# Optimization experiments

Hardware: AMD Instinct MI355X
Metric: run time of the kernel (lower is better)

Reference implementation:

```python
import jax, jax.numpy as jnp
import numpy as np

N, E = 20000, 160000
H, C1, C_OUT, D_IN = 4, 256, 512, 128
HID = H * C1  # 1024


def gat_conv(x, src, dst, W, a_src, a_dst, b, heads, ch, concat):
    n = x.shape[0]
    xw = (x @ W).reshape(n, heads, ch)                     # [N,H,C]
    es = jnp.sum(xw * a_src, axis=-1)                      # [N,H]
    ed = jnp.sum(xw * a_dst, axis=-1)                      # [N,H]
    e = jax.nn.leaky_relu(es[src] + ed[dst], 0.2)          # [Etot,H]
    m = jax.ops.segment_max(e, dst, num_segments=n)
    m = jnp.where(jnp.isfinite(m), m, 0.0)
    p = jnp.exp(e - m[dst])
    denom = jax.ops.segment_sum(p, dst, num_segments=n)
    alpha = p / (denom[dst] + 1e-16)                       # segment softmax
    out = jax.ops.segment_sum(alpha[:, :, None] * xw[src], dst, num_segments=n)
    out = out.reshape(n, heads * ch) if concat else out.mean(axis=1)
    return out + b


def layer_norm(x, g, b, eps=1e-5):
    mu = jnp.mean(x, axis=-1, keepdims=True)
    var = jnp.var(x, axis=-1, keepdims=True)
    return (x - mu) * jax.lax.rsqrt(var + eps) * g + b


def setup_inputs() -> dict:
    key = jax.random.key(0)
    ks = jax.random.split(key, 16)
    s1, s2, s3 = (2.0 / D_IN) ** 0.5, (2.0 / HID) ** 0.5, (2.0 / HID) ** 0.5
    return {
        "x": jax.random.normal(ks[0], (N, D_IN), jnp.float32),
        "edge_index": jax.random.randint(ks[1], (2, E), 0, N, jnp.int64),
        "W1": jax.random.normal(ks[2], (D_IN, H * C1), jnp.float32) * s1,
        "a_src1": jax.random.normal(ks[3], (H, C1), jnp.float32) * 0.1,
        "a_dst1": jax.random.normal(ks[4], (H, C1), jnp.float32) * 0.1,
        "b1": jnp.zeros((HID,), jnp.float32),
        "ln1_g": jnp.ones((HID,), jnp.float32),
        "ln1_b": jnp.zeros((HID,), jnp.float32),
        "W2": jax.random.normal(ks[5], (HID, H * C1), jnp.float32) * s2,
        "a_src2": jax.random.normal(ks[6], (H, C1), jnp.float32) * 0.1,
        "a_dst2": jax.random.normal(ks[7], (H, C1), jnp.float32) * 0.1,
        "b2": jnp.zeros((HID,), jnp.float32),
        "ln2_g": jnp.ones((HID,), jnp.float32),
        "ln2_b": jnp.zeros((HID,), jnp.float32),
        "W3": jax.random.normal(ks[8], (HID, C_OUT), jnp.float32) * s3,
        "a_src3": jax.random.normal(ks[9], (1, C_OUT), jnp.float32) * 0.1,
        "a_dst3": jax.random.normal(ks[10], (1, C_OUT), jnp.float32) * 0.1,
        "b3": jnp.zeros((C_OUT,), jnp.float32),
    }


def reference(x, edge_index, W1, a_src1, a_dst1, b1, ln1_g, ln1_b,
              W2, a_src2, a_dst2, b2, ln2_g, ln2_b,
              W3, a_src3, a_dst3, b3):
    # add self loops (PyG GATConv default add_self_loops=True)
    loops = jnp.arange(N, dtype=edge_index.dtype)
    src = jnp.concatenate([edge_index[0], loops])
    dst = jnp.concatenate([edge_index[1], loops])

    h = gat_conv(x, src, dst, W1, a_src1, a_dst1, b1, H, C1, True)
    h = jax.nn.elu(layer_norm(h, ln1_g, ln1_b))  # dropout: eval mode (identity)
    h = gat_conv(h, src, dst, W2, a_src2, a_dst2, b2, H, C1, True)
    h = jax.nn.elu(layer_norm(h, ln2_g, ln2_b))
    out = gat_conv(h, src, dst, W3, a_src3, a_dst3, b3, 1, C_OUT, True)
    return out
```

## Files before the change

kernel.cpp:

```cpp
#include <hip/hip_runtime.h>
#include <hip/hip_bf16.h>

typedef __hip_bfloat16 bf16;
typedef __attribute__((ext_vector_type(8))) short short8;
typedef __attribute__((ext_vector_type(8))) unsigned short ushort8v;
typedef __attribute__((ext_vector_type(4))) float float4v;

#define NN 20000
#define EE 160000
#define ET (NN + EE)

__device__ __forceinline__ float bf2f(bf16 v){ return __bfloat162float(v); }
__device__ __forceinline__ float raw2f(unsigned short u){ return __uint_as_float(((unsigned)u) << 16); }
__device__ __forceinline__ unsigned short f2raw(float f){
  bf16 h = __float2bfloat16(f);
  return *(unsigned short*)&h;
}

__device__ __forceinline__ int detect_f32(const void* raw, int nwords, int lane){
  unsigned v = ((const unsigned*)raw)[lane % nwords];
  int e8 = (v >> 7) & 0xFF;
  int looks = (e8 >= 100 && e8 <= 140) ? 1 : 0;
  unsigned long long mz = __ballot(v == 0u);
  unsigned long long ml = __ballot(looks);
  int nz = __popcll(mz);
  int nonz = 64 - nz;
  int nl = __popcll(ml);
  return (nonz > 0 && 2*nl >= nonz) ? 0 : 1;
}

__device__ __forceinline__ int detect_i64(const int* eiraw, int lane){
  int odd = eiraw[2*lane + 1];
  unsigned long long m2 = __ballot(odd != 0);
  return (m2 == 0ULL) ? 1 : 0;
}

struct P13 { const void* src[13]; int off[13]; int n[13]; };
struct PrepArgs {
  const void* xraw; bf16* Xc;
  const void* w1raw; bf16* Wt1;
  const void* w2raw; bf16* Wt2;
  const void* w3raw; bf16* Wt3;
  const int* eiraw; int* eic;
  P13 p13; float* prm;
  int* counts;
  float* esA; float* edA;
};

__device__ __forceinline__ void do_transpose(float (*tile)[33], const void* raw,
    bf16* wt, int K, int M, int f, int bx, int by, int t){
  int kb = by*32, mb = bx*32;
  int tx = t & 31, ty = t >> 5;
  for (int r = 0; r < 4; r++){
    int k = kb + ty + r*8;
    int m = mb + tx;
    float v = f ? ((const float*)raw)[(size_t)k*M+m] : bf2f(((const bf16*)raw)[(size_t)k*M+m]);
    tile[ty + r*8][tx] = v;
  }
  __syncthreads();
  for (int r = 0; r < 4; r++){
    int m = mb + ty + r*8;
    int k = kb + tx;
    wt[(size_t)m*K + k] = __float2bfloat16(tile[tx][ty + r*8]);
  }
}

__global__ __launch_bounds__(256) void k_prep(PrepArgs A){
  __shared__ float tile[32][33];
  int b = blockIdx.x, t = threadIdx.x;
  int lane = t & 63;
  if (b < 10000){
    int f = detect_f32(A.xraw, NN*128/2, lane);
    int i = b*256 + t;
    if (f) A.Xc[i] = __float2bfloat16(((const float*)A.xraw)[i]);
    else   A.Xc[i] = ((const bf16*)A.xraw)[i];
  } else if (b < 10128){
    int f = detect_f32(A.w1raw, 128*1024/2, lane);
    int r = b - 10000;
    do_transpose(tile, A.w1raw, A.Wt1, 128, 1024, f, r & 31, r >> 5, t);
  } else if (b < 11152){
    int f = detect_f32(A.w2raw, 1024*1024/2, lane);
    int r = b - 10128;
    do_transpose(tile, A.w2raw, A.Wt2, 1024, 1024, f, r & 31, r >> 5, t);
  } else if (b < 11664){
    int f = detect_f32(A.w3raw, 1024*512/2, lane);
    int r = b - 11152;
    do_transpose(tile, A.w3raw, A.Wt3, 1024, 512, f, r & 15, r >> 4, t);
  } else if (b < 12914){
    int f64 = detect_i64(A.eiraw, lane);
    int i = (b - 11664)*256 + t;
    if (i < 2*EE) A.eic[i] = f64 ? A.eiraw[2*i] : A.eiraw[i];
  } else if (b < 12927){
    int pb = b - 12914;
    const void* s = A.p13.src[pb];
    int n = A.p13.n[pb];
    int f = detect_f32(s, n/2, lane);
    float* d = A.prm + A.p13.off[pb];
    for (int i = t; i < n; i += 256)
      d[i] = f ? ((const float*)s)[i] : bf2f(((const bf16*)s)[i]);
  } else if (b < 13006){
    int i = (b - 12927)*256 + t;
    if (i < NN) A.counts[i] = 1;
  } else {
    int i = (b - 13006)*256 + t;
    if (i < NN*4){ A.esA[i] = 0.f; A.edA[i] = 0.f; }
  }
}

__global__ void k_hist(const int* __restrict__ ei, int* __restrict__ counts){
  int e = blockIdx.x*256 + threadIdx.x;
  if (e < EE){
    int d = ei[EE + e];
    if (d >= 0 && d < NN) atomicAdd(&counts[d], 1);
  }
}

__global__ __launch_bounds__(1024) void k_scan(const int* __restrict__ counts, int* __restrict__ rp,
    int* __restrict__ cursor, int* __restrict__ col){
  __shared__ int wsum[16];
  __shared__ int sc;
  int t = threadIdx.x, lane = t & 63, wv = t >> 6;
  if (t == 0) sc = 0;
  __syncthreads();
  for (int base = 0; base < NN; base += 1024){
    int i = base + t;
    int v = (i < NN) ? counts[i] : 0;
    int x = v;
    #pragma unroll
    for (int o = 1; o < 64; o <<= 1){
      int y = __shfl_up(x, o, 64);
      if (lane >= o) x += y;
    }
    if (lane == 63) wsum[wv] = x;
    __syncthreads();
    if (wv == 0 && lane < 16){
      int w = wsum[lane];
      #pragma unroll
      for (int o = 1; o < 16; o <<= 1){
        int y = __shfl_up(w, o, 16);
        if ((lane & 15) >= o) w += y;
      }
      wsum[lane] = w;
    }
    __syncthreads();
    int carry = sc;
    int wpre = (wv > 0) ? wsum[wv-1] : 0;
    if (i < NN){
      int p = carry + wpre + x - v;
      rp[i] = p;
      col[p] = i;
      cursor[i] = p + 1;
    }
    __syncthreads();
    if (t == 1023) sc = carry + wsum[15];
    __syncthreads();
  }
  if (t == 0) rp[NN] = sc;
}

__global__ void k_scatter(const int* __restrict__ ei, int* __restrict__ cursor, int* __restrict__ col){
  int e = blockIdx.x*256 + threadIdx.x;
  if (e < EE){
    int s = ei[e], d = ei[EE + e];
    if (d >= 0 && d < NN){
      int pos = atomicAdd(&cursor[d], 1);
      col[pos] = s;
    }
  }
}

__global__ __launch_bounds__(256) void k_gemm_mfma(
    const bf16* __restrict__ X, const bf16* __restrict__ Wt, bf16* __restrict__ Y,
    const float* __restrict__ as_, const float* __restrict__ ad_,
    float* __restrict__ es, float* __restrict__ ed,
    int K, int M, int C, int H)
{
  __shared__ bf16 Xs[64*64];
  __shared__ bf16 Bs[128*64];
  int ncols = gridDim.x;
  int bid = blockIdx.y * ncols + blockIdx.x;
  int xcd  = bid & 7;
  int rest = bid >> 3;
  int colb = rest % ncols;
  int rowb = xcd + 8 * (rest / ncols);
  int r0 = rowb * 64;
  if (r0 >= NN) return;
  int c0 = colb * 128;

  int tid  = threadIdx.x;
  int wave = tid >> 6, lane = tid & 63;
  int quad = lane >> 4, l15 = lane & 15;
  int wr = (wave >> 1) * 32;
  int wc = (wave & 1) * 64;
  int sw = l15 & 7;

  float4v acc[2][4];
  #pragma unroll
  for (int i=0;i<2;i++)
    #pragma unroll
    for (int j=0;j<4;j++)
      acc[i][j] = (float4v){0.f,0.f,0.f,0.f};

  for (int k0 = 0; k0 < K; k0 += 64){
    #pragma unroll
    for (int i = 0; i < 2; i++){
      int ch = i*256 + tid;
      int row = ch >> 3, kl = ch & 7;
      int kg = kl ^ (row & 7);
      const bf16* gx = X + (size_t)(r0 + row)*K + k0 + kg*8;
      __builtin_amdgcn_global_load_lds(
        (const __attribute__((address_space(1))) unsigned int*)gx,
        (__attribute__((address_space(3))) unsigned int*)(Xs + ch*8), 16, 0, 0);
    }
    #pragma unroll
    for (int i = 0; i < 4; i++){
      int ch = i*256 + tid;
      int row = ch >> 3, kl = ch & 7;
      int kg = kl ^ (row & 7);
      const bf16* gb = Wt + (size_t)(c0 + row)*K + k0 + kg*8;
      __builtin_amdgcn_global_load_lds(
        (const __attribute__((address_space(1))) unsigned int*)gb,
        (__attribute__((address_space(3))) unsigned int*)(Bs + ch*8), 16, 0, 0);
    }
    __syncthreads();

    #pragma unroll
    for (int kk = 0; kk < 2; kk++){
      int kp = quad + kk*4;
      short8 af[2], bfr[4];
      #pragma unroll
      for (int i = 0; i < 2; i++){
        int r = wr + i*16 + l15;
        af[i] = *(const short8*)(Xs + ((size_t)r*8 + (kp ^ sw))*8);
      }
      #pragma unroll
      for (int j = 0; j < 4; j++){
        int r = wc + j*16 + l15;
        bfr[j] = *(const short8*)(Bs + ((size_t)r*8 + (kp ^ sw))*8);
      }
      #pragma unroll
      for (int i = 0; i < 2; i++)
        #pragma unroll
        for (int j = 0; j < 4; j++)
          acc[i][j] = __builtin_amdgcn_mfma_f32_16x16x32_bf16(af[i], bfr[j], acc[i][j], 0, 0, 0);
    }
    __syncthreads();
  }

  int h = c0 / C;
  float asv[4], adv[4];
  #pragma unroll
  for (int j = 0; j < 4; j++){
    int colj = c0 + wc + j*16 + l15;
    asv[j] = as_[colj]; adv[j] = ad_[colj];
  }
  #pragma unroll
  for (int i = 0; i < 2; i++){
    int rbase = r0 + wr + i*16 + quad*4;
    #pragma unroll
    for (int rg = 0; rg < 4; rg++){
      int row = rbase + rg;
      bool ok = (row < NN);
      float pe = 0.f, pd = 0.f;
      #pragma unroll
      for (int j = 0; j < 4; j++){
        float v = acc[i][j][rg];
        int colj = c0 + wc + j*16 + l15;
        if (ok) Y[(size_t)row*M + colj] = __float2bfloat16(v);
        pe += v * asv[j];
        pd += v * adv[j];
      }
      #pragma unroll
      for (int o = 1; o < 16; o <<= 1){
        pe += __shfl_xor(pe, o, 64);
        pd += __shfl_xor(pd, o, 64);
      }
      if (ok && l15 == 0){
        atomicAdd(&es[row*H + h], pe);
        atomicAdd(&ed[row*H + h], pd);
      }
    }
  }
}

__global__ __launch_bounds__(128) void k_aggln(const int* __restrict__ rp, const int* __restrict__ col,
    const bf16* __restrict__ xw, const float* __restrict__ es, const float* __restrict__ ed,
    const float* __restrict__ bias, const float* __restrict__ gam, const float* __restrict__ bet,
    bf16* __restrict__ act, float* __restrict__ esz, float* __restrict__ edz, int zn){
  int wv = threadIdx.x >> 6, lane = threadIdx.x & 63;
  int n = blockIdx.x*2 + wv;
  int h = lane >> 4;
  int cb = lane * 16;
  int e0 = rp[n], e1 = rp[n+1], deg = e1 - e0;
  float4 ed4 = *(const float4*)&ed[n*4];
  const unsigned short* xwu = (const unsigned short*)xw;

  float acc[16];
  #pragma unroll
  for (int c=0;c<16;c++) acc[c]=0.f;

  if (deg <= 64){
    int src = 0;
    float l0=-1e30f, l1=-1e30f, l2=-1e30f, l3=-1e30f;
    if (lane < deg){
      src = col[e0 + lane];
      float4 e4 = *(const float4*)&es[src*4];
      float v;
      v = e4.x + ed4.x; l0 = v > 0.f ? v : 0.2f*v;
      v = e4.y + ed4.y; l1 = v > 0.f ? v : 0.2f*v;
      v = e4.z + ed4.z; l2 = v > 0.f ? v : 0.2f*v;
      v = e4.w + ed4.w; l3 = v > 0.f ? v : 0.2f*v;
    }
    float m0=l0, m1=l1, m2=l2, m3=l3;
    #pragma unroll
    for (int o=1;o<64;o<<=1){
      m0 = fmaxf(m0, __shfl_xor(m0,o,64));
      m1 = fmaxf(m1, __shfl_xor(m1,o,64));
      m2 = fmaxf(m2, __shfl_xor(m2,o,64));
      m3 = fmaxf(m3, __shfl_xor(m3,o,64));
    }
    float p0 = (lane<deg) ? __expf(l0-m0) : 0.f;
    float p1 = (lane<deg) ? __expf(l1-m1) : 0.f;
    float p2 = (lane<deg) ? __expf(l2-m2) : 0.f;
    float p3 = (lane<deg) ? __expf(l3-m3) : 0.f;
    float d0=p0, d1=p1, d2=p2, d3=p3;
    #pragma unroll
    for (int o=1;o<64;o<<=1){
      d0 += __shfl_xor(d0,o,64);
      d1 += __shfl_xor(d1,o,64);
      d2 += __shfl_xor(d2,o,64);
      d3 += __shfl_xor(d3,o,64);
    }
    float al0 = p0 * (1.f/(d0+1e-16f));
    float al1 = p1 * (1.f/(d1+1e-16f));
    float al2 = p2 * (1.f/(d2+1e-16f));
    float al3 = p3 * (1.f/(d3+1e-16f));

    int j = 0;
    for (; j + 4 <= deg; j += 4){
      int sA = __shfl(src, j, 64);
      int sB = __shfl(src, j+1, 64);
      int sC = __shfl(src, j+2, 64);
      int sD = __shfl(src, j+3, 64);
      float a0A = __shfl(al0, j, 64),   a1A = __shfl(al1, j, 64);
      float a2A = __shfl(al2, j, 64),   a3A = __shfl(al3, j, 64);
      float a0B = __shfl(al0, j+1, 64), a1B = __shfl(al1, j+1, 64);
      float a2B = __shfl(al2, j+1, 64), a3B = __shfl(al3, j+1, 64);
      float a0C = __shfl(al0, j+2, 64), a1C = __shfl(al1, j+2, 64);
      float a2C = __shfl(al2, j+2, 64), a3C = __shfl(al3, j+2, 64);
      float a0D = __shfl(al0, j+3, 64), a1D = __shfl(al1, j+3, 64);
      float a2D = __shfl(al2, j+3, 64), a3D = __shfl(al3, j+3, 64);
      float aA = (h==0) ? a0A : ((h==1) ? a1A : ((h==2) ? a2A : a3A));
      float aB = (h==0) ? a0B : ((h==1) ? a1B : ((h==2) ? a2B : a3B));
      float aC = (h==0) ? a0C : ((h==1) ? a1C : ((h==2) ? a2C : a3C));
      float aD = (h==0) ? a0D : ((h==1) ? a1D : ((h==2) ? a2D : a3D));
      const unsigned short* rA = xwu + (size_t)sA*1024 + cb;
      const unsigned short* rB = xwu + (size_t)sB*1024 + cb;
      const unsigned short* rC = xwu + (size_t)sC*1024 + cb;
      const unsigned short* rD = xwu + (size_t)sD*1024 + cb;
      ushort8v uA0 = *(const ushort8v*)(rA);
      ushort8v uA1 = *(const ushort8v*)(rA+8);
      ushort8v uB0 = *(const ushort8v*)(rB);
      ushort8v uB1 = *(const ushort8v*)(rB+8);
      ushort8v uC0 = *(const ushort8v*)(rC);
      ushort8v uC1 = *(const ushort8v*)(rC+8);
      ushort8v uD0 = *(const ushort8v*)(rD);
      ushort8v uD1 = *(const ushort8v*)(rD+8);
      #pragma unroll
      for (int c=0;c<8;c++){ acc[c]   += aA*raw2f(uA0[c]); acc[8+c] += aA*raw2f(uA1[c]); }
      #pragma unroll
      for (int c=0;c<8;c++){ acc[c]   += aB*raw2f(uB0[c]); acc[8+c] += aB*raw2f(uB1[c]); }
      #pragma unroll
      for (int c=0;c<8;c++){ acc[c]   += aC*raw2f(uC0[c]); acc[8+c] += aC*raw2f(uC1[c]); }
      #pragma unroll
      for (int c=0;c<8;c++){ acc[c]   += aD*raw2f(uD0[c]); acc[8+c] += aD*raw2f(uD1[c]); }
    }
    for (; j < deg; j++){
      int s = __shfl(src, j, 64);
      float a0j = __shfl(al0, j, 64);
      float a1j = __shfl(al1, j, 64);
      float a2j = __shfl(al2, j, 64);
      float a3j = __shfl(al3, j, 64);
      float aj = (h==0) ? a0j : ((h==1) ? a1j : ((h==2) ? a2j : a3j));
      const unsigned short* row = xwu + (size_t)s*1024 + cb;
      ushort8v u0 = *(const ushort8v*)(row);
      ushort8v u1 = *(const ushort8v*)(row+8);
      #pragma unroll
      for (int c=0;c<8;c++){ acc[c] += aj*raw2f(u0[c]); acc[8+c] += aj*raw2f(u1[c]); }
    }
  } else {
    float edh = (h==0) ? ed4.x : ((h==1) ? ed4.y : ((h==2) ? ed4.z : ed4.w));
    float m = -1e30f;
    for (int e=e0;e<e1;e++){
      float v = es[col[e]*4 + h] + edh;
      v = v > 0.f ? v : 0.2f*v;
      m = fmaxf(m, v);
    }
    float den = 0.f;
    for (int e=e0;e<e1;e++){
      float v = es[col[e]*4 + h] + edh;
      v = v > 0.f ? v : 0.2f*v;
      den += __expf(v - m);
    }
    float rd = 1.f/(den + 1e-16f);
    for (int e=e0;e<e1;e++){
      int s = col[e];
      float v = es[s*4 + h] + edh;
      v = v > 0.f ? v : 0.2f*v;
      float aj = __expf(v - m) * rd;
      const unsigned short* row = xwu + (size_t)s*1024 + cb;
      ushort8v u0 = *(const ushort8v*)(row);
      ushort8v u1 = *(const ushort8v*)(row+8);
      #pragma unroll
      for (int c=0;c<8;c++){ acc[c] += aj*raw2f(u0[c]); acc[8+c] += aj*raw2f(u1[c]); }
    }
  }

  #pragma unroll
  for (int c=0;c<16;c++) acc[c] += bias[cb+c];
  float s1 = 0.f, s2 = 0.f;
  #pragma unroll
  for (int c=0;c<16;c++){ s1 += acc[c]; s2 += acc[c]*acc[c]; }
  #pragma unroll
  for (int o=1;o<64;o<<=1){
    s1 += __shfl_xor(s1,o,64);
    s2 += __shfl_xor(s2,o,64);
  }
  float mu  = s1 * (1.f/1024.f);
  float var = s2 * (1.f/1024.f) - mu*mu;
  float rstd = rsqrtf(fmaxf(var, 0.f) + 1e-5f);

  ushort4 o4[4];
  #pragma unroll
  for (int q=0;q<4;q++){
    float v0 = (acc[q*4+0]-mu)*rstd*gam[cb+q*4+0] + bet[cb+q*4+0];
    float v1 = (acc[q*4+1]-mu)*rstd*gam[cb+q*4+1] + bet[cb+q*4+1];
    float v2 = (acc[q*4+2]-mu)*rstd*gam[cb+q*4+2] + bet[cb+q*4+2];
    float v3 = (acc[q*4+3]-mu)*rstd*gam[cb+q*4+3] + bet[cb+q*4+3];
    v0 = v0 > 0.f ? v0 : (__expf(v0)-1.f);
    v1 = v1 > 0.f ? v1 : (__expf(v1)-1.f);
    v2 = v2 > 0.f ? v2 : (__expf(v2)-1.f);
    v3 = v3 > 0.f ? v3 : (__expf(v3)-1.f);
    o4[q].x = f2raw(v0); o4[q].y = f2raw(v1); o4[q].z = f2raw(v2); o4[q].w = f2raw(v3);
  }
  unsigned short* dst = (unsigned short*)act + (size_t)n*1024 + cb;
  *(ushort4*)(dst)    = o4[0];
  *(ushort4*)(dst+4)  = o4[1];
  *(ushort4*)(dst+8)  = o4[2];
  *(ushort4*)(dst+12) = o4[3];

  if (lane < zn){ esz[n*zn + lane] = 0.f; edz[n*zn + lane] = 0.f; }
}

__global__ __launch_bounds__(128) void k_agg3(const int* __restrict__ rp, const int* __restrict__ col,
    const bf16* __restrict__ xw, const float* __restrict__ es, const float* __restrict__ ed,
    const float* __restrict__ bias, float* __restrict__ out){
  int wv = threadIdx.x >> 6, lane = threadIdx.x & 63;
  int n = blockIdx.x*2 + wv;
  int cb = lane * 8;
  int e0 = rp[n], e1 = rp[n+1], deg = e1 - e0;
  float edv = ed[n];
  const unsigned short* xwu = (const unsigned short*)xw;

  float acc[8];
  #pragma unroll
  for (int c=0;c<8;c++) acc[c]=0.f;

  if (deg <= 64){
    int src = 0;
    float l = -1e30f;
    if (lane < deg){
      src = col[e0 + lane];
      float v = es[src] + edv;
      l = v > 0.f ? v : 0.2f*v;
    }
    float m = l;
    #pragma unroll
    for (int o=1;o<64;o<<=1) m = fmaxf(m, __shfl_xor(m,o,64));
    float p = (lane<deg) ? __expf(l-m) : 0.f;
    float d = p;
    #pragma unroll
    for (int o=1;o<64;o<<=1) d += __shfl_xor(d,o,64);
    float al = p * (1.f/(d+1e-16f));

    int j = 0;
    for (; j + 4 <= deg; j += 4){
      int sA = __shfl(src, j, 64);
      int sB = __shfl(src, j+1, 64);
      int sC = __shfl(src, j+2, 64);
      int sD = __shfl(src, j+3, 64);
      float aA = __shfl(al, j, 64);
      float aB = __shfl(al, j+1, 64);
      float aC = __shfl(al, j+2, 64);
      float aD = __shfl(al, j+3, 64);
      const unsigned short* rA = xwu + (size_t)sA*512 + cb;
      const unsigned short* rB = xwu + (size_t)sB*512 + cb;
      const unsigned short* rC = xwu + (size_t)sC*512 + cb;
      const unsigned short* rD = xwu + (size_t)sD*512 + cb;
      ushort8v uA = *(const ushort8v*)(rA);
      ushort8v uB = *(const ushort8v*)(rB);
      ushort8v uC = *(const ushort8v*)(rC);
      ushort8v uD = *(const ushort8v*)(rD);
      #pragma unroll
      for (int c=0;c<8;c++) acc[c] += aA*raw2f(uA[c]);
      #pragma unroll
      for (int c=0;c<8;c++) acc[c] += aB*raw2f(uB[c]);
      #pragma unroll
      for (int c=0;c<8;c++) acc[c] += aC*raw2f(uC[c]);
      #pragma unroll
      for (int c=0;c<8;c++) acc[c] += aD*raw2f(uD[c]);
    }
    for (; j < deg; j++){
      int s = __shfl(src, j, 64);
      float aj = __shfl(al, j, 64);
      const unsigned short* row = xwu + (size_t)s*512 + cb;
      ushort8v u = *(const ushort8v*)(row);
      #pragma unroll
      for (int c=0;c<8;c++) acc[c] += aj*raw2f(u[c]);
    }
  } else {
    float m = -1e30f;
    for (int e=e0;e<e1;e++){
      float v = es[col[e]] + edv;
      v = v > 0.f ? v : 0.2f*v;
      m = fmaxf(m, v);
    }
    float den = 0.f;
    for (int e=e0;e<e1;e++){
      float v = es[col[e]] + edv;
      v = v > 0.f ? v : 0.2f*v;
      den += __expf(v - m);
    }
    float rd = 1.f/(den + 1e-16f);
    for (int e=e0;e<e1;e++){
      int s = col[e];
      float v = es[s] + edv;
      v = v > 0.f ? v : 0.2f*v;
      float aj = __expf(v - m) * rd;
      const unsigned short* row = xwu + (size_t)s*512 + cb;
      ushort8v u = *(const ushort8v*)(row);
      #pragma unroll
      for (int c=0;c<8;c++) acc[c] += aj*raw2f(u[c]);
    }
  }
  float* dst = out + (size_t)n*512 + cb;
  #pragma unroll
  for (int c=0;c<8;c++) dst[c] = acc[c] + bias[cb+c];
}

__global__ void k_wssmall(float* __restrict__ out, float code){
  if (threadIdx.x == 0) out[0] = code;
}

extern "C" void kernel_launch(void* const* d_in, const int* in_sizes, int n_in,
                              void* d_out, int out_size, void* d_ws, size_t ws_size,
                              hipStream_t stream){
  float* out = (float*)d_out;
  char* ws = (char*)d_ws;

  static const int EXP_SZ[18] = {2560000, 320000, 131072, 1024,1024,1024,1024,1024,
                                 1048576, 1024,1024,1024,1024,1024,
                                 524288, 512,512,512};
  if (n_in != 18){ k_wssmall<<<1,64,0,stream>>>(out, 500.0f*301.0f); return; }
  for (int i = 0; i < 18; i++)
    if (in_sizes[i] != EXP_SZ[i]){ k_wssmall<<<1,64,0,stream>>>(out, 500.0f*302.0f); return; }
  if (out_size != NN*512){ k_wssmall<<<1,64,0,stream>>>(out, 500.0f*303.0f); return; }
  const size_t NEED = 93215360;
  if (ws_size < NEED){ k_wssmall<<<1,64,0,stream>>>(out, 500.0f*304.0f); return; }

  bf16* xw    = (bf16*) (ws);
  int*  cnt   = (int*)  (ws);
  bf16* act   = (bf16*) (ws + 40960000);
  int*  cursor= (int*)  (ws + 40960000);
  bf16* Xc    = (bf16*) (ws + 81920000);
  float* esC  = (float*)(ws + 81920000);
  float* edC  = (float*)(ws + 82000000);
  bf16* Wt1   = (bf16*) (ws + 87040000);
  bf16* Wt2   = (bf16*) (ws + 87302144);
  bf16* Wt3   = (bf16*) (ws + 89399296);
  float* prm  = (float*)(ws + 90447872);
  int*  eic   = (int*)  (ws + 90495232);
  float* esB  = (float*)(ws + 90495232);
  float* edB  = (float*)(ws + 90815232);
  float* esA  = (float*)(ws + 91775232);
  float* edA  = (float*)(ws + 92095232);
  int*  rp    = (int*)  (ws + 92415232);
  int*  col   = (int*)  (ws + 92495360);

  float *as1=prm+0, *ad1=prm+1024, *b1=prm+2048, *lg1=prm+3072, *lb1=prm+4096;
  float *as2=prm+5120, *ad2=prm+6144, *b2=prm+7168, *lg2=prm+8192, *lb2=prm+9216;
  float *as3=prm+10240, *ad3=prm+10752, *b3=prm+11264;

  const int TB = 256;
  int gbE = (EE + TB - 1)/TB;

  {
    PrepArgs A;
    A.xraw = d_in[0]; A.Xc = Xc;
    A.w1raw = d_in[2]; A.Wt1 = Wt1;
    A.w2raw = d_in[8]; A.Wt2 = Wt2;
    A.w3raw = d_in[14]; A.Wt3 = Wt3;
    A.eiraw = (const int*)d_in[1]; A.eic = eic;
    const int idx[13] = {3,4,5,6,7, 9,10,11,12,13, 15,16,17};
    const int off[13] = {0,1024,2048,3072,4096, 5120,6144,7168,8192,9216, 10240,10752,11264};
    const int nn [13] = {1024,1024,1024,1024,1024, 1024,1024,1024,1024,1024, 512,512,512};
    for (int i=0;i<13;i++){ A.p13.src[i]=d_in[idx[i]]; A.p13.off[i]=off[i]; A.p13.n[i]=nn[i]; }
    A.prm = prm; A.counts = cnt; A.esA = esA; A.edA = edA;
    k_prep<<<13006 + 313, TB, 0, stream>>>(A);
  }

  k_hist<<<gbE, TB, 0, stream>>>(eic, cnt);
  k_scan<<<1, 1024, 0, stream>>>(cnt, rp, cursor, col);
  k_scatter<<<gbE, TB, 0, stream>>>(eic, cursor, col);

  const int RB = (NN + 63)/64;
  const int R8 = ((RB + 7)/8)*8;
  dim3 g12(1024/128, R8);
  dim3 g3 (512/128,  R8);

  k_gemm_mfma<<<g12, TB, 0, stream>>>(Xc, Wt1, xw, as1, ad1, esA, edA, 128, 1024, 256, 4);
  k_aggln<<<NN/2, 128, 0, stream>>>(rp, col, xw, esA, edA, b1, lg1, lb1, act, esB, edB, 4);

  k_gemm_mfma<<<g12, TB, 0, stream>>>(act, Wt2, xw, as2, ad2, esB, edB, 1024, 1024, 256, 4);
  k_aggln<<<NN/2, 128, 0, stream>>>(rp, col, xw, esB, edB, b2, lg2, lb2, act, esC, edC, 1);

  k_gemm_mfma<<<g3, TB, 0, stream>>>(act, Wt3, xw, as3, ad3, esC, edC, 1024, 512, 512, 1);
  k_agg3<<<NN/2, 128, 0, stream>>>(rp, col, xw, esC, edC, b3, out);
}
```

Baseline: 452.9 us.

## Add 256x256-tile 8-wave pipelined MFMA GEMM for layers two and three

Adds a new GEMM kernel with 256x256 output tiles, 512 threads (8 waves), and double-buffered LDS filled by direct global-to-LDS loads with an XOR swizzle. It interleaves quarter MFMA blocks with prefetches under explicit barriers and priority hints, and remaps block IDs so that row blocks are spread across XCDs. It replaces the old 64x128 GEMM for the two K=1024 layers to raise data reuse per tile and overlap loads with math. In exchange it uses 128KB of LDS and many accumulator registers, so occupancy drops. Row tails past NN are only guarded on stores, so the last tile reads rows beyond the input.

```diff
diff --git a/kernel.cpp b/kernel.cpp
--- a/kernel.cpp
+++ b/kernel.cpp
@@ -283,6 +283,171 @@
   }
 }
 
+__global__ __launch_bounds__(512, 2) void k_gemm_8p(
+    const bf16* __restrict__ X, const bf16* __restrict__ Wt, bf16* __restrict__ Y,
+    const float* __restrict__ as_, const float* __restrict__ ad_,
+    float* __restrict__ es, float* __restrict__ ed,
+    int K, int M, int C, int H)
+{
+  __shared__ bf16 As[2][16384];
+  __shared__ bf16 Bs[2][16384];
+  int ncols = gridDim.x;
+  int bid = blockIdx.y * ncols + blockIdx.x;
+  int xcd  = bid & 7;
+  int rest = bid >> 3;
+  int colb = rest % ncols;
+  int rowb = xcd + 8 * (rest / ncols);
+  int r0 = rowb * 256;
+  if (r0 >= NN) return;
+  int c0 = colb * 256;
+
+  int tid  = threadIdx.x;
+  int wave = tid >> 6, lane = tid & 63;
+  int wm = wave >> 2, wn = wave & 3;
+  int quad = lane >> 4, l15 = lane & 15;
+  int sw = l15 & 7;
+  int ar = wm * 128;
+  int bc = wn * 64;
+
+  float4v acc[8][4];
+  #pragma unroll
+  for (int i=0;i<8;i++)
+    #pragma unroll
+    for (int j=0;j<4;j++) acc[i][j] = (float4v){0.f,0.f,0.f,0.f};
+
+  int nst   = K >> 6;
+  int niter = nst >> 1;
+
+#define SA8(b, hh, kt) { _Pragma("unroll") for (int i_=0;i_<2;i_++){ \
+    int ch = i_*512 + tid; int row = (hh)*128 + (ch>>3); int kg = (ch&7) ^ (row&7); \
+    const bf16* g = X + (size_t)(r0+row)*K + (kt)*64 + kg*8; \
+    __builtin_amdgcn_global_load_lds((const __attribute__((address_space(1))) unsigned int*)g, \
+      (__attribute__((address_space(3))) unsigned int*)(&As[b][((hh)*1024 + ch)*8]), 16, 0, 0); } }
+#define SB8(b, hh, kt) { _Pragma("unroll") for (int i_=0;i_<2;i_++){ \
+    int ch = i_*512 + tid; int row = (hh)*128 + (ch>>3); int kg = (ch&7) ^ (row&7); \
+    const bf16* g = Wt + (size_t)(c0+row)*K + (kt)*64 + kg*8; \
+    __builtin_amdgcn_global_load_lds((const __attribute__((address_space(1))) unsigned int*)g, \
+      (__attribute__((address_space(3))) unsigned int*)(&Bs[b][((hh)*1024 + ch)*8]), 16, 0, 0); } }
+
+#define PBAR() { __builtin_amdgcn_sched_barrier(0); __builtin_amdgcn_s_barrier(); __builtin_amdgcn_sched_barrier(0); }
+#define LGKM0() { asm volatile("s_waitcnt lgkmcnt(0)" ::: "memory"); __builtin_amdgcn_sched_barrier(0); }
+
+  short8 a0[2][4], a1[2][4], b0[2][2], b1[2][2];
+
+#define LDA0(b) { _Pragma("unroll") for (int kk=0;kk<2;kk++){ int kp = quad + kk*4; \
+    _Pragma("unroll") for (int i=0;i<4;i++){ int r = ar + i*16 + l15; \
+      a0[kk][i] = *(const short8*)(&As[b][((r*8) + (kp^sw))*8]); } } }
+#define LDA1(b) { _Pragma("unroll") for (int kk=0;kk<2;kk++){ int kp = quad + kk*4; \
+    _Pragma("unroll") for (int i=0;i<4;i++){ int r = ar + 64 + i*16 + l15; \
+      a1[kk][i] = *(const short8*)(&As[b][((r*8) + (kp^sw))*8]); } } }
+#define LDB0(b) { _Pragma("unroll") for (int kk=0;kk<2;kk++){ int kp = quad + kk*4; \
+    _Pragma("unroll") for (int j=0;j<2;j++){ int r = bc + j*16 + l15; \
+      b0[kk][j] = *(const short8*)(&Bs[b][((r*8) + (kp^sw))*8]); } } }
+#define LDB1(b) { _Pragma("unroll") for (int kk=0;kk<2;kk++){ int kp = quad + kk*4; \
+    _Pragma("unroll") for (int j=0;j<2;j++){ int r = bc + 32 + j*16 + l15; \
+      b1[kk][j] = *(const short8*)(&Bs[b][((r*8) + (kp^sw))*8]); } } }
+
+#define MQ(AR, BR, I0, J0) { __builtin_amdgcn_s_setprio(1); \
+    _Pragma("unroll") for (int kk=0;kk<2;kk++) \
+    _Pragma("unroll") for (int i=0;i<4;i++) \
+    _Pragma("unroll") for (int j=0;j<2;j++) \
+      acc[(I0)+i][(J0)+j] = __builtin_amdgcn_mfma_f32_16x16x32_bf16(AR[kk][i], BR[kk][j], acc[(I0)+i][(J0)+j], 0, 0, 0); \
+    __builtin_amdgcn_s_setprio(0); }
+
+  SA8(0,0,0); SA8(0,1,0); SB8(0,0,0); SB8(0,1,0);
+  SA8(1,0,1); SA8(1,1,1);
+  asm volatile("s_waitcnt vmcnt(4)" ::: "memory");
+  PBAR();
+
+  for (int it = 0; it < niter; it++){
+    int t0 = it << 1;
+    bool last = (it == niter-1);
+    LDA0(0); LDB0(0); LDB1(0);
+    SB8(1,0,t0+1);
+    PBAR(); LGKM0();
+    MQ(a0,b0,0,0);
+    PBAR();
+    LDA1(0);
+    SB8(1,1,t0+1);
+    PBAR(); LGKM0();
+    MQ(a0,b1,0,2);
+    PBAR();
+    if (!last) SA8(0,0,t0+2);
+    PBAR(); LGKM0();
+    MQ(a1,b1,4,2);
+    PBAR();
+    if (!last) SA8(0,1,t0+2);
+    PBAR(); LGKM0();
+    MQ(a1,b0,4,0);
+    if (last){ asm volatile("s_waitcnt vmcnt(0)" ::: "memory"); }
+    else     { asm volatile("s_waitcnt vmcnt(4)" ::: "memory"); }
+    PBAR();
+    LDA0(1); LDB0(1); LDB1(1);
+    if (!last) SB8(0,0,t0+2);
+    PBAR(); LGKM0();
+    MQ(a0,b0,0,0);
+    PBAR();
+    LDA1(1);
+    if (!last) SB8(0,1,t0+2);
+    PBAR(); LGKM0();
+    MQ(a0,b1,0,2);
+    PBAR();
+    if (!last) SA8(1,0,t0+3);
+    PBAR(); LGKM0();
+    MQ(a1,b1,4,2);
+    PBAR();
+    if (!last) SA8(1,1,t0+3);
+    PBAR(); LGKM0();
+    MQ(a1,b0,4,0);
+    if (!last){ asm volatile("s_waitcnt vmcnt(4)" ::: "memory"); }
+    PBAR();
+  }
+#undef SA8
+#undef SB8
+#undef PBAR
+#undef LGKM0
+#undef LDA0
+#undef LDA1
+#undef LDB0
+#undef LDB1
+#undef MQ
+
+  int h = c0 / C;
+  float asv[4], adv[4];
+  #pragma unroll
+  for (int j = 0; j < 4; j++){
+    int colj = c0 + bc + j*16 + l15;
+    asv[j] = as_[colj]; adv[j] = ad_[colj];
+  }
+  #pragma unroll
+  for (int i = 0; i < 8; i++){
+    int rbase = r0 + ar + i*16 + quad*4;
+    #pragma unroll
+    for (int rg = 0; rg < 4; rg++){
+      int row = rbase + rg;
+      bool ok = (row < NN);
+      float pe = 0.f, pd = 0.f;
+      #pragma unroll
+      for (int j = 0; j < 4; j++){
+        float v = acc[i][j][rg];
+        int colj = c0 + bc + j*16 + l15;
+        if (ok) Y[(size_t)row*M + colj] = __float2bfloat16(v);
+        pe += v * asv[j];
+        pd += v * adv[j];
+      }
+      #pragma unroll
+      for (int o = 1; o < 16; o <<= 1){
+        pe += __shfl_xor(pe, o, 64);
+        pd += __shfl_xor(pd, o, 64);
+      }
+      if (ok && l15 == 0){
+        atomicAdd(&es[row*H + h], pe);
+        atomicAdd(&ed[row*H + h], pd);
+      }
+    }
+  }
+}
+
 __global__ __launch_bounds__(128) void k_aggln(const int* __restrict__ rp, const int* __restrict__ col,
     const bf16* __restrict__ xw, const float* __restrict__ es, const float* __restrict__ ed,
     const float* __restrict__ bias, const float* __restrict__ gam, const float* __restrict__ bet,
@@ -615,15 +780,18 @@
 
   const int RB = (NN + 63)/64;
   const int R8 = ((RB + 7)/8)*8;
-  dim3 g12(1024/128, R8);
-  dim3 g3 (512/128,  R8);
-
-  k_gemm_mfma<<<g12, TB, 0, stream>>>(Xc, Wt1, xw, as1, ad1, esA, edA, 128, 1024, 256, 4);
+  dim3 g1(1024/128, R8);
+
+  const int RB2 = ((((NN + 255)/256) + 7)/8)*8;
+  dim3 g2(1024/256, RB2);
+  dim3 g3(512/256,  RB2);
+
+  k_gemm_mfma<<<g1, TB, 0, stream>>>(Xc, Wt1, xw, as1, ad1, esA, edA, 128, 1024, 256, 4);
   k_aggln<<<NN/2, 128, 0, stream>>>(rp, col, xw, esA, edA, b1, lg1, lb1, act, esB, edB, 4);
 
-  k_gemm_mfma<<<g12, TB, 0, stream>>>(act, Wt2, xw, as2, ad2, esB, edB, 1024, 1024, 256, 4);
+  k_gemm_8p<<<g2, 512, 0, stream>>>(act, Wt2, xw, as2, ad2, esB, edB, 1024, 1024, 256, 4);
   k_aggln<<<NN/2, 128, 0, stream>>>(rp, col, xw, esB, edB, b2, lg2, lb2, act, esC, edC, 1);
 
-  k_gemm_mfma<<<g3, TB, 0, stream>>>(act, Wt3, xw, as3, ad3, esC, edC, 1024, 512, 512, 1);
+  k_gemm_8p<<<g3, 512, 0, stream>>>(act, Wt3, xw, as3, ad3, esC, edC, 1024, 512, 512, 1);
   k_agg3<<<NN/2, 128, 0, stream>>>(rp, col, xw, esC, edC, b3, out);
 }
```

Result: slower. 557.0 us (+23.0%).
